# Kernel tuning notes

Measured on AMD Instinct MI355X. Metric: run time of the kernel, lower is better.

## Reference

```python
import jax, jax.numpy as jnp
import numpy as np

B, H, C_LEN, Q_LEN = 64, 128, 1024, 128


def setup_inputs() -> dict:
    key = jax.random.key(0)
    k1, k2, k3 = jax.random.split(key, 3)
    context = jax.random.normal(k1, (B, H, C_LEN), dtype=jnp.float32)
    question = jax.random.normal(k2, (B, H, Q_LEN), dtype=jnp.float32)
    lim = np.sqrt(1.0 / H)
    w = jax.random.uniform(k3, (3 * H,), dtype=jnp.float32, minval=-lim, maxval=lim)
    return {"context": context, "question": question, "w": w}


def reference(context, question, w):
    # context: (B, H, C), question: (B, H, Q); w: (3H,) with cat order (q, c, cq)
    h = w.shape[0] // 3
    w_q, w_c, w_cq = w[:h], w[h:2 * h], w[2 * h:]
    c = jnp.transpose(context, (0, 2, 1))   # (B, C, H)
    q = jnp.transpose(question, (0, 2, 1))  # (B, Q, H)
    # trilinear similarity s[b,i,j] = c_i.w_c + q_j.w_q + (c_i*w_cq).q_j  -> (B, C, Q)
    s = (c @ w_c)[:, :, None] + (q @ w_q)[:, None, :] \
        + jnp.einsum('bih,bjh->bij', c * w_cq, q)
    # original applies softmax over dim=1 (context axis) for BOTH s1 and s2
    s1 = jax.nn.softmax(s, axis=1)           # (B, C, Q)
    a = jnp.einsum('bij,bjh->bih', s1, q)    # (B, C, H)
    l = jnp.einsum('bij,bkj->bik', s1, s1)   # (B, C, C)
    b = jnp.einsum('bik,bkh->bih', l, c)     # (B, C, H)
    out = jnp.concatenate([c, a, c * a, c * b], axis=2)  # (B, C, 4H)
    # dropout disabled (drop_prob=0) for deterministic reference
    return jnp.transpose(out, (0, 2, 1))     # (B, 4H, C)
```

## Files before the change

kernel.cpp:

```cpp
#include <hip/hip_runtime.h>

#define BB 64
#define HH 128
#define CC 1024
#define QQ 128

typedef unsigned short u16;
typedef unsigned int u32;
using bf16x8 = __attribute__((ext_vector_type(8))) short;
using f32x4 = __attribute__((ext_vector_type(4))) float;

#define MFMA16(a, b, c) __builtin_amdgcn_mfma_f32_16x16x32_bf16(a, b, c, 0, 0, 0)

__device__ __forceinline__ float lo2f(u32 u) {
  union { float f; u32 i; } v; v.i = u << 16; return v.f;
}
__device__ __forceinline__ float hi2f(u32 u) {
  union { float f; u32 i; } v; v.i = u & 0xFFFF0000u; return v.f;
}
__device__ __forceinline__ u16 f2b(float f) {
  union { float f; u32 i; } v; v.f = f;
  u32 r = v.i + 0x7FFFu + ((v.i >> 16) & 1u);
  return (u16)(r >> 16);
}
__device__ __forceinline__ u32 pack_hi2(float a, float b) {
  return (__float_as_uint(a) >> 16) | (__float_as_uint(b) & 0xFFFF0000u);
}
__device__ __forceinline__ u32 pack_lo2(float a, float b) {
  float ra = a - __uint_as_float(__float_as_uint(a) & 0xFFFF0000u);
  float rb = b - __uint_as_float(__float_as_uint(b) & 0xFFFF0000u);
  return (__float_as_uint(ra) >> 16) | (__float_as_uint(rb) & 0xFFFF0000u);
}

__device__ __forceinline__ void stage16(const float* __restrict__ p,
                                        u16* dhi, u16* dlo) {
  float4 a0 = *(const float4*)p;
  float4 a1 = *(const float4*)(p + 4);
  float4 a2 = *(const float4*)(p + 8);
  float4 a3 = *(const float4*)(p + 12);
  uint4 h0 = {pack_hi2(a0.x, a0.y), pack_hi2(a0.z, a0.w),
              pack_hi2(a1.x, a1.y), pack_hi2(a1.z, a1.w)};
  uint4 h1 = {pack_hi2(a2.x, a2.y), pack_hi2(a2.z, a2.w),
              pack_hi2(a3.x, a3.y), pack_hi2(a3.z, a3.w)};
  uint4 l0 = {pack_lo2(a0.x, a0.y), pack_lo2(a0.z, a0.w),
              pack_lo2(a1.x, a1.y), pack_lo2(a1.z, a1.w)};
  uint4 l1 = {pack_lo2(a2.x, a2.y), pack_lo2(a2.z, a2.w),
              pack_lo2(a3.x, a3.y), pack_lo2(a3.z, a3.w)};
  *(uint4*)dhi = h0;
  *(uint4*)(dhi + 8) = h1;
  *(uint4*)dlo = l0;
  *(uint4*)(dlo + 8) = l1;
}

__global__ __launch_bounds__(512) void k1_s_softmax(
    const float* __restrict__ ctx, const float* __restrict__ qst,
    const float* __restrict__ w, u16* __restrict__ s1ws,
    u16* __restrict__ s1tb) {
  const int b = blockIdx.x;
  const int j0 = blockIdx.y * 16;
  const int tid = threadIdx.x;
  const float* cb = ctx + (size_t)b * HH * CC;
  const float* qb = qst + (size_t)b * HH * QQ;

  float dotv[16][2];
  float qwq[16];
  float cwc[2] = {0.f, 0.f};
#pragma unroll
  for (int jj = 0; jj < 16; ++jj) {
    qwq[jj] = 0.f;
    dotv[jj][0] = dotv[jj][1] = 0.f;
  }

  for (int h = 0; h < HH; ++h) {
    const float2 cv = *(const float2*)(cb + (size_t)h * CC + tid * 2);
    float c0 = cv.x, c1 = cv.y;
    float wqv = w[h], wcv = w[HH + h], wcqv = w[2 * HH + h];
    cwc[0] += c0 * wcv; cwc[1] += c1 * wcv;
    float t0 = c0 * wcqv, t1 = c1 * wcqv;
    const float4* qrow = (const float4*)(qb + (size_t)h * QQ + j0);
    float4 q0 = qrow[0], q1 = qrow[1], q2 = qrow[2], q3 = qrow[3];
    float qv[16] = {q0.x, q0.y, q0.z, q0.w, q1.x, q1.y, q1.z, q1.w,
                    q2.x, q2.y, q2.z, q2.w, q3.x, q3.y, q3.z, q3.w};
#pragma unroll
    for (int jj = 0; jj < 16; ++jj) {
      qwq[jj] += qv[jj] * wqv;
      dotv[jj][0] += t0 * qv[jj];
      dotv[jj][1] += t1 * qv[jj];
    }
  }
#pragma unroll
  for (int jj = 0; jj < 16; ++jj) {
    float base = qwq[jj];
    dotv[jj][0] += cwc[0] + base;
    dotv[jj][1] += cwc[1] + base;
  }

  __shared__ float red[16 * 512];
  __shared__ float red2[16 * 32];
  __shared__ float bc[16];
  const int rj = tid >> 5, rs = tid & 31;

#pragma unroll
  for (int jj = 0; jj < 16; ++jj)
    red[jj * 512 + tid] = fmaxf(dotv[jj][0], dotv[jj][1]);
  __syncthreads();
  {
    float m = red[rj * 512 + rs * 16];
#pragma unroll
    for (int g = 1; g < 16; ++g) m = fmaxf(m, red[rj * 512 + rs * 16 + g]);
    red2[rj * 32 + rs] = m;
  }
  __syncthreads();
  if (tid < 16) {
    float m = red2[tid * 32];
#pragma unroll
    for (int g = 1; g < 32; ++g) m = fmaxf(m, red2[tid * 32 + g]);
    bc[tid] = m;
  }
  __syncthreads();

#pragma unroll
  for (int jj = 0; jj < 16; ++jj) {
    float mj = bc[jj];
    float e0 = __expf(dotv[jj][0] - mj);
    float e1 = __expf(dotv[jj][1] - mj);
    dotv[jj][0] = e0; dotv[jj][1] = e1;
    red[jj * 512 + tid] = e0 + e1;
  }
  __syncthreads();
  {
    float s = 0.f;
#pragma unroll
    for (int g = 0; g < 16; ++g) s += red[rj * 512 + rs * 16 + g];
    red2[rj * 32 + rs] = s;
  }
  __syncthreads();
  if (tid < 16) {
    float s = 0.f;
#pragma unroll
    for (int g = 0; g < 32; ++g) s += red2[tid * 32 + g];
    bc[tid] = 1.0f / s;
  }
  __syncthreads();

#pragma unroll
  for (int jj = 0; jj < 16; ++jj) {
    float inv = bc[jj];
    dotv[jj][0] *= inv;
    dotv[jj][1] *= inv;
  }
  u16* srow = s1ws + ((size_t)b * QQ + j0) * CC + tid * 2;
#pragma unroll
  for (int jj = 0; jj < 16; ++jj) {
    u32 pk = (u32)f2b(dotv[jj][0]) | ((u32)f2b(dotv[jj][1]) << 16);
    *(u32*)(srow + (size_t)jj * CC) = pk;
  }
  u16* stb = s1tb + (size_t)b * (16 * 1024 * 8);
  const int jg0 = j0 >> 3;
#pragma unroll
  for (int g = 0; g < 2; ++g) {
#pragma unroll
    for (int rr = 0; rr < 2; ++rr) {
      const int o = g * 8;
      uint4 v;
      v.x = (u32)f2b(dotv[o + 0][rr]) | ((u32)f2b(dotv[o + 1][rr]) << 16);
      v.y = (u32)f2b(dotv[o + 2][rr]) | ((u32)f2b(dotv[o + 3][rr]) << 16);
      v.z = (u32)f2b(dotv[o + 4][rr]) | ((u32)f2b(dotv[o + 5][rr]) << 16);
      v.w = (u32)f2b(dotv[o + 6][rr]) | ((u32)f2b(dotv[o + 7][rr]) << 16);
      *(uint4*)(stb + ((size_t)(jg0 + g) * 1024 + (tid * 2 + rr)) * 8) = v;
    }
  }
}

__global__ __launch_bounds__(256, 2) void k2_t(
    const float* __restrict__ ctx, const u16* __restrict__ s1ws,
    float* __restrict__ tT) {
  const int b = blockIdx.x;
  const int kz = blockIdx.y;
  const int tid = threadIdx.x;
  const int lane = tid & 63;
  const int wv = tid >> 6;
  const int l15 = lane & 15, l4 = lane >> 4;

  __shared__ u16 sHi[128 * 32];
  __shared__ u16 sLo[128 * 32];

  f32x4 acc[2][8];
#pragma unroll
  for (int ht = 0; ht < 2; ++ht)
#pragma unroll
    for (int jt = 0; jt < 8; ++jt) acc[ht][jt] = 0.f;

  const float* cb = ctx + (size_t)b * HH * CC;
  const u16* sb = s1ws + (size_t)b * QQ * CC;
  const int srow = tid >> 1;
  const int scol = (tid & 1) * 16;

  for (int ks = 0; ks < 4; ++ks) {
    const int ib = kz * 128 + ks * 32;
    __syncthreads();
    stage16(cb + (size_t)srow * CC + ib + scol,
            &sHi[srow * 32 + scol], &sLo[srow * 32 + scol]);
    __syncthreads();
    bf16x8 aHi[2], aLo[2];
#pragma unroll
    for (int ht = 0; ht < 2; ++ht) {
      const int ar = (wv * 32 + ht * 16 + l15) * 32 + l4 * 8;
      aHi[ht] = *(const bf16x8*)&sHi[ar];
      aLo[ht] = *(const bf16x8*)&sLo[ar];
    }
#pragma unroll
    for (int jt = 0; jt < 8; ++jt) {
      bf16x8 bf =
          *(const bf16x8*)(sb + (size_t)(jt * 16 + l15) * CC + ib + l4 * 8);
#pragma unroll
      for (int ht = 0; ht < 2; ++ht) {
        acc[ht][jt] = MFMA16(aHi[ht], bf, acc[ht][jt]);
        acc[ht][jt] = MFMA16(aLo[ht], bf, acc[ht][jt]);
      }
    }
  }
  float* tb = tT + (size_t)b * HH * QQ;
#pragma unroll
  for (int ht = 0; ht < 2; ++ht)
#pragma unroll
    for (int jt = 0; jt < 8; ++jt)
#pragma unroll
      for (int r = 0; r < 4; ++r) {
        const int h = wv * 32 + ht * 16 + l4 * 4 + r;
        const int j = jt * 16 + l15;
        atomicAdd(&tb[(size_t)h * QQ + j], acc[ht][jt][r]);
      }
}

__global__ __launch_bounds__(256, 2) void k3_out(
    const float* __restrict__ ctx, const float* __restrict__ qst,
    const u16* __restrict__ s1tb, const float* __restrict__ tT,
    float* __restrict__ out) {
  const int b = blockIdx.x;
  const int i0 = blockIdx.y * 128;
  const int tid = threadIdx.x;
  const int lane = tid & 63;
  const int wv = tid >> 6;
  const int l15 = lane & 15, l4 = lane >> 4;

  __shared__ u16 qHi[128 * 32], qLo[128 * 32];
  __shared__ u16 tHi[128 * 32], tLo[128 * 32];

  f32x4 accA[8][2], accB[8][2];
#pragma unroll
  for (int it = 0; it < 8; ++it)
#pragma unroll
    for (int ht = 0; ht < 2; ++ht) { accA[it][ht] = 0.f; accB[it][ht] = 0.f; }

  const u16* stb = s1tb + (size_t)b * (16 * 1024 * 8);
  const float* qb = qst + (size_t)b * HH * QQ;
  const float* tb = tT + (size_t)b * HH * QQ;
  const int srow = tid >> 1;
  const int scol = (tid & 1) * 16;

  for (int ks = 0; ks < 4; ++ks) {
    const int jb = ks * 32;
    __syncthreads();
    stage16(qb + (size_t)srow * QQ + jb + scol,
            &qHi[srow * 32 + scol], &qLo[srow * 32 + scol]);
    stage16(tb + (size_t)srow * QQ + jb + scol,
            &tHi[srow * 32 + scol], &tLo[srow * 32 + scol]);
    __syncthreads();
    bf16x8 qh[2], ql[2], th[2], tl[2];
#pragma unroll
    for (int ht = 0; ht < 2; ++ht) {
      const int ar = (wv * 32 + ht * 16 + l15) * 32 + l4 * 8;
      qh[ht] = *(const bf16x8*)&qHi[ar];
      ql[ht] = *(const bf16x8*)&qLo[ar];
      th[ht] = *(const bf16x8*)&tHi[ar];
      tl[ht] = *(const bf16x8*)&tLo[ar];
    }
#pragma unroll
    for (int half = 0; half < 2; ++half) {
      bf16x8 af[4];
#pragma unroll
      for (int t4 = 0; t4 < 4; ++t4) {
        const int it = half * 4 + t4;
        af[t4] = *(const bf16x8*)(stb +
            ((size_t)(ks * 4 + l4) * 1024 + i0 + it * 16 + l15) * 8);
      }
#pragma unroll
      for (int t4 = 0; t4 < 4; ++t4) {
        const int it = half * 4 + t4;
#pragma unroll
        for (int ht = 0; ht < 2; ++ht) {
          accA[it][ht] = MFMA16(af[t4], qh[ht], accA[it][ht]);
          accA[it][ht] = MFMA16(af[t4], ql[ht], accA[it][ht]);
          accB[it][ht] = MFMA16(af[t4], th[ht], accB[it][ht]);
          accB[it][ht] = MFMA16(af[t4], tl[ht], accB[it][ht]);
        }
      }
    }
  }

  const float* cb = ctx + (size_t)b * HH * CC;
  float* ob = out + (size_t)b * 4 * HH * CC;
#pragma unroll
  for (int it = 0; it < 8; ++it)
#pragma unroll
    for (int ht = 0; ht < 2; ++ht) {
      const int h = wv * 32 + ht * 16 + l15;
      const int ii = i0 + it * 16 + l4 * 4;
      float4 cv = *(const float4*)(cb + (size_t)h * CC + ii);
      f32x4 aA = accA[it][ht], aB = accB[it][ht];
      float4 oA = {aA[0], aA[1], aA[2], aA[3]};
      float4 cA = {cv.x * oA.x, cv.y * oA.y, cv.z * oA.z, cv.w * oA.w};
      float4 cB = {cv.x * aB[0], cv.y * aB[1], cv.z * aB[2], cv.w * aB[3]};
      const size_t base = (size_t)h * CC + ii;
      *(float4*)(ob + base) = cv;
      *(float4*)(ob + (size_t)HH * CC + base) = oA;
      *(float4*)(ob + (size_t)2 * HH * CC + base) = cA;
      *(float4*)(ob + (size_t)3 * HH * CC + base) = cB;
    }
}

extern "C" void kernel_launch(void* const* d_in, const int* in_sizes, int n_in,
                              void* d_out, int out_size, void* d_ws, size_t ws_size,
                              hipStream_t stream) {
  const float* ctx = (const float*)d_in[0];
  const float* qst = (const float*)d_in[1];
  const float* w = (const float*)d_in[2];
  for (int k = 0; k < n_in; ++k) {
    if (in_sizes[k] == BB * HH * CC) ctx = (const float*)d_in[k];
    else if (in_sizes[k] == BB * HH * QQ) qst = (const float*)d_in[k];
    else if (in_sizes[k] == 3 * HH) w = (const float*)d_in[k];
  }
  float* out = (float*)d_out;

  u16* s1ws = (u16*)d_ws;
  u16* s1tb = (u16*)((char*)d_ws + (size_t)16 * 1024 * 1024);
  float* tT = (float*)((char*)d_ws + (size_t)32 * 1024 * 1024);

  k1_s_softmax<<<dim3(BB, QQ / 16), 512, 0, stream>>>(ctx, qst, w, s1ws, s1tb);
  hipMemsetAsync(tT, 0, (size_t)BB * QQ * HH * sizeof(float), stream);
  k2_t<<<dim3(BB, 8), 256, 0, stream>>>(ctx, s1ws, tT);
  k3_out<<<dim3(BB, 8), 256, 0, stream>>>(ctx, qst, s1tb, tT, out);
}
```

Before: 271.8 us.

## Retile k2 over output tiles to drop split-K atomics and memset, pad k3 LDS

k2_t now assigns each block a 32x64 output tile of T over the full context length instead of splitting K across blocks, so results are written directly and the atomicAdd epilogue plus the preceding memset go away. Context is staged in 128-wide padded LDS tiles. In k3_out the LDS rows are padded to reduce bank conflicts, and the MFMA operand order is swapped so each lane owns one context column and stores scalars with coalesced column access. The trade-off is that each k2 block rereads context over the full length with fewer MFMAs per sync, and k3 now issues scalar stores instead of float4 stores.

```diff
diff --git a/kernel.cpp b/kernel.cpp
--- a/kernel.cpp
+++ b/kernel.cpp
@@ -172,65 +172,53 @@
   }
 }
 
-__global__ __launch_bounds__(256, 2) void k2_t(
+__global__ __launch_bounds__(256) void k2_t(
     const float* __restrict__ ctx, const u16* __restrict__ s1ws,
     float* __restrict__ tT) {
   const int b = blockIdx.x;
-  const int kz = blockIdx.y;
+  const int h0 = (blockIdx.y >> 1) * 32;
+  const int j0 = (blockIdx.y & 1) * 64;
   const int tid = threadIdx.x;
   const int lane = tid & 63;
   const int wv = tid >> 6;
   const int l15 = lane & 15, l4 = lane >> 4;
 
-  __shared__ u16 sHi[128 * 32];
-  __shared__ u16 sLo[128 * 32];
-
-  f32x4 acc[2][8];
+  __shared__ u16 sHi[32 * 136];
+  __shared__ u16 sLo[32 * 136];
+
+  f32x4 acc[2];
+  acc[0] = 0.f; acc[1] = 0.f;
+
+  const float* cb = ctx + ((size_t)b * HH + h0) * CC;
+  const u16* sb = s1ws + ((size_t)b * QQ + j0 + wv * 16 + l15) * CC;
+  const int srow = tid >> 3;
+  const int scol = (tid & 7) * 16;
+
+  for (int k0 = 0; k0 < CC; k0 += 128) {
+    __syncthreads();
+    stage16(cb + (size_t)srow * CC + k0 + scol,
+            &sHi[srow * 136 + scol], &sLo[srow * 136 + scol]);
+    __syncthreads();
+#pragma unroll
+    for (int kk = 0; kk < 4; ++kk) {
+      bf16x8 bf = *(const bf16x8*)(sb + k0 + kk * 32 + l4 * 8);
+#pragma unroll
+      for (int ht = 0; ht < 2; ++ht) {
+        const int ar = (ht * 16 + l15) * 136 + kk * 32 + l4 * 8;
+        bf16x8 ah = *(const bf16x8*)&sHi[ar];
+        bf16x8 al = *(const bf16x8*)&sLo[ar];
+        acc[ht] = MFMA16(ah, bf, acc[ht]);
+        acc[ht] = MFMA16(al, bf, acc[ht]);
+      }
+    }
+  }
+  float* tb = tT + (size_t)b * HH * QQ;
 #pragma unroll
   for (int ht = 0; ht < 2; ++ht)
 #pragma unroll
-    for (int jt = 0; jt < 8; ++jt) acc[ht][jt] = 0.f;
-
-  const float* cb = ctx + (size_t)b * HH * CC;
-  const u16* sb = s1ws + (size_t)b * QQ * CC;
-  const int srow = tid >> 1;
-  const int scol = (tid & 1) * 16;
-
-  for (int ks = 0; ks < 4; ++ks) {
-    const int ib = kz * 128 + ks * 32;
-    __syncthreads();
-    stage16(cb + (size_t)srow * CC + ib + scol,
-            &sHi[srow * 32 + scol], &sLo[srow * 32 + scol]);
-    __syncthreads();
-    bf16x8 aHi[2], aLo[2];
-#pragma unroll
-    for (int ht = 0; ht < 2; ++ht) {
-      const int ar = (wv * 32 + ht * 16 + l15) * 32 + l4 * 8;
-      aHi[ht] = *(const bf16x8*)&sHi[ar];
-      aLo[ht] = *(const bf16x8*)&sLo[ar];
-    }
-#pragma unroll
-    for (int jt = 0; jt < 8; ++jt) {
-      bf16x8 bf =
-          *(const bf16x8*)(sb + (size_t)(jt * 16 + l15) * CC + ib + l4 * 8);
-#pragma unroll
-      for (int ht = 0; ht < 2; ++ht) {
-        acc[ht][jt] = MFMA16(aHi[ht], bf, acc[ht][jt]);
-        acc[ht][jt] = MFMA16(aLo[ht], bf, acc[ht][jt]);
-      }
-    }
-  }
-  float* tb = tT + (size_t)b * HH * QQ;
-#pragma unroll
-  for (int ht = 0; ht < 2; ++ht)
-#pragma unroll
-    for (int jt = 0; jt < 8; ++jt)
-#pragma unroll
-      for (int r = 0; r < 4; ++r) {
-        const int h = wv * 32 + ht * 16 + l4 * 4 + r;
-        const int j = jt * 16 + l15;
-        atomicAdd(&tb[(size_t)h * QQ + j], acc[ht][jt][r]);
-      }
+    for (int r = 0; r < 4; ++r)
+      tb[(size_t)(h0 + ht * 16 + l4 * 4 + r) * QQ + j0 + wv * 16 + l15] =
+          acc[ht][r];
 }
 
 __global__ __launch_bounds__(256, 2) void k3_out(
@@ -244,8 +232,8 @@
   const int wv = tid >> 6;
   const int l15 = lane & 15, l4 = lane >> 4;
 
-  __shared__ u16 qHi[128 * 32], qLo[128 * 32];
-  __shared__ u16 tHi[128 * 32], tLo[128 * 32];
+  __shared__ u16 qHi[128 * 40], qLo[128 * 40];
+  __shared__ u16 tHi[128 * 40], tLo[128 * 40];
 
   f32x4 accA[8][2], accB[8][2];
 #pragma unroll
@@ -263,14 +251,14 @@
     const int jb = ks * 32;
     __syncthreads();
     stage16(qb + (size_t)srow * QQ + jb + scol,
-            &qHi[srow * 32 + scol], &qLo[srow * 32 + scol]);
+            &qHi[srow * 40 + scol], &qLo[srow * 40 + scol]);
     stage16(tb + (size_t)srow * QQ + jb + scol,
-            &tHi[srow * 32 + scol], &tLo[srow * 32 + scol]);
+            &tHi[srow * 40 + scol], &tLo[srow * 40 + scol]);
     __syncthreads();
     bf16x8 qh[2], ql[2], th[2], tl[2];
 #pragma unroll
     for (int ht = 0; ht < 2; ++ht) {
-      const int ar = (wv * 32 + ht * 16 + l15) * 32 + l4 * 8;
+      const int ar = (wv * 32 + ht * 16 + l15) * 40 + l4 * 8;
       qh[ht] = *(const bf16x8*)&qHi[ar];
       ql[ht] = *(const bf16x8*)&qLo[ar];
       th[ht] = *(const bf16x8*)&tHi[ar];
@@ -278,11 +266,11 @@
     }
 #pragma unroll
     for (int half = 0; half < 2; ++half) {
-      bf16x8 af[4];
+      bf16x8 bfr[4];
 #pragma unroll
       for (int t4 = 0; t4 < 4; ++t4) {
         const int it = half * 4 + t4;
-        af[t4] = *(const bf16x8*)(stb +
+        bfr[t4] = *(const bf16x8*)(stb +
             ((size_t)(ks * 4 + l4) * 1024 + i0 + it * 16 + l15) * 8);
       }
 #pragma unroll
@@ -290,10 +278,10 @@
         const int it = half * 4 + t4;
 #pragma unroll
         for (int ht = 0; ht < 2; ++ht) {
-          accA[it][ht] = MFMA16(af[t4], qh[ht], accA[it][ht]);
-          accA[it][ht] = MFMA16(af[t4], ql[ht], accA[it][ht]);
-          accB[it][ht] = MFMA16(af[t4], th[ht], accB[it][ht]);
-          accB[it][ht] = MFMA16(af[t4], tl[ht], accB[it][ht]);
+          accA[it][ht] = MFMA16(qh[ht], bfr[t4], accA[it][ht]);
+          accA[it][ht] = MFMA16(ql[ht], bfr[t4], accA[it][ht]);
+          accB[it][ht] = MFMA16(th[ht], bfr[t4], accB[it][ht]);
+          accB[it][ht] = MFMA16(tl[ht], bfr[t4], accB[it][ht]);
         }
       }
     }
@@ -302,22 +290,24 @@
   const float* cb = ctx + (size_t)b * HH * CC;
   float* ob = out + (size_t)b * 4 * HH * CC;
 #pragma unroll
-  for (int it = 0; it < 8; ++it)
+  for (int it = 0; it < 8; ++it) {
+    const int ii = i0 + it * 16 + l15;
 #pragma unroll
     for (int ht = 0; ht < 2; ++ht) {
-      const int h = wv * 32 + ht * 16 + l15;
-      const int ii = i0 + it * 16 + l4 * 4;
-      float4 cv = *(const float4*)(cb + (size_t)h * CC + ii);
-      f32x4 aA = accA[it][ht], aB = accB[it][ht];
-      float4 oA = {aA[0], aA[1], aA[2], aA[3]};
-      float4 cA = {cv.x * oA.x, cv.y * oA.y, cv.z * oA.z, cv.w * oA.w};
-      float4 cB = {cv.x * aB[0], cv.y * aB[1], cv.z * aB[2], cv.w * aB[3]};
-      const size_t base = (size_t)h * CC + ii;
-      *(float4*)(ob + base) = cv;
-      *(float4*)(ob + (size_t)HH * CC + base) = oA;
-      *(float4*)(ob + (size_t)2 * HH * CC + base) = cA;
-      *(float4*)(ob + (size_t)3 * HH * CC + base) = cB;
-    }
+#pragma unroll
+      for (int r = 0; r < 4; ++r) {
+        const int h = wv * 32 + ht * 16 + l4 * 4 + r;
+        const size_t base = (size_t)h * CC + ii;
+        const float cv = cb[base];
+        const float av = accA[it][ht][r];
+        const float bv = accB[it][ht][r];
+        ob[base] = cv;
+        ob[(size_t)HH * CC + base] = av;
+        ob[(size_t)2 * HH * CC + base] = cv * av;
+        ob[(size_t)3 * HH * CC + base] = cv * bv;
+      }
+    }
+  }
 }
 
 extern "C" void kernel_launch(void* const* d_in, const int* in_sizes, int n_in,
@@ -338,7 +328,6 @@
   float* tT = (float*)((char*)d_ws + (size_t)32 * 1024 * 1024);
 
   k1_s_softmax<<<dim3(BB, QQ / 16), 512, 0, stream>>>(ctx, qst, w, s1ws, s1tb);
-  hipMemsetAsync(tT, 0, (size_t)BB * QQ * HH * sizeof(float), stream);
   k2_t<<<dim3(BB, 8), 256, 0, stream>>>(ctx, s1ws, tT);
   k3_out<<<dim3(BB, 8), 256, 0, stream>>>(ctx, qst, s1tb, tT, out);
 }
```

After: 250.9 us. 1.08x faster.
